# Kernel optimization log

Measured on AMD Instinct MI355X. Metric: run time of the kernel, lower is better.

Reference implementation:

```python
import jax, jax.numpy as jnp
import numpy as np

B, CIN, COUT, H, W, KH, KW, G = 16, 64, 128, 128, 128, 3, 3, 4


def setup_inputs() -> dict:
    key = jax.random.key(0)
    k1, k2, k3 = jax.random.split(key, 3)
    x = jax.random.normal(k1, (B, CIN, H, W), dtype=jnp.float32)
    spline_weights = jax.random.normal(k2, (COUT, CIN, KH, KW, G), dtype=jnp.float32)
    basis_weights = jax.random.normal(k3, (COUT, CIN, KH, KW), dtype=jnp.float32)
    return {"x": x, "spline_weights": spline_weights, "basis_weights": basis_weights}


def _conv_same(inp, w):
    # NCHW x OIHW -> NCHW, stride 1, SAME padding (pad = k//2, matches torch F.pad)
    return jax.lax.conv_general_dilated(
        inp, w, window_strides=(1, 1),
        padding=[(KH // 2, KH // 2), (KW // 2, KW // 2)],
        dimension_numbers=("NCHW", "OIHW", "NCHW"))


def reference(x, spline_weights, basis_weights):
    # spline branch: patch broadcast over grid then summed == conv with grid-summed kernel
    w_spline = spline_weights.sum(axis=-1)  # (COUT, CIN, KH, KW)
    # basis branch: silu applied to (zero-)padded patches; silu(0)=0 so equals conv(silu(x))
    return _conv_same(x, w_spline) + _conv_same(jax.nn.silu(x), basis_weights)
```

## Files before the change

kernel.cpp:

```cpp
#include <hip/hip_runtime.h>
#include <math.h>

#define B_    16
#define CIN   64
#define COUT  128
#define H_    128
#define W_    128
#define CI2   128
#define KTOT  1152

typedef __bf16 bf16x8 __attribute__((ext_vector_type(8)));
typedef float  f32x4  __attribute__((ext_vector_type(4)));

#define XT_BYTES  ((size_t)B_ * H_ * W_ * CI2 * 2)
#define WC_BYTES  ((size_t)COUT * KTOT * 2)
#define Z_OFF     (XT_BYTES + WC_BYTES)
#define WS_NEED   (Z_OFF + 4096)

__global__ __launch_bounds__(256) void w_prep(const float* __restrict__ sw,
                                              const float* __restrict__ bw,
                                              __bf16* __restrict__ wc,
                                              float* __restrict__ zp) {
    const int i = blockIdx.x * 256 + threadIdx.x;
    if (blockIdx.x == 0) zp[threadIdx.x] = 0.f;
    if (i >= COUT * KTOT) return;
    const int co = i / KTOT, k = i - co * KTOT;
    const int tap = k >> 7, ci2 = k & 127;
    float v;
    if (ci2 < CIN) {
        const float* p = sw + ((size_t)(co * CIN + ci2) * 9 + tap) * 4;
        v = p[0] + p[1] + p[2] + p[3];
    } else {
        v = bw[(size_t)(co * CIN + (ci2 - CIN)) * 9 + tap];
    }
    const int wm = co >> 6, m = (co >> 4) & 3, l15 = co & 15;
    const int ks = ci2 >> 5, lq = (ci2 >> 3) & 3, e = ci2 & 7;
    const int qq = (ks >> 1) * 18 + tap * 2 + (ks & 1);
    const int f  = wm * 4 + m;
    const size_t off = ((size_t)(qq * 8 + f)) * 512 + (lq * 16 + l15) * 8 + e;
    wc[off] = (__bf16)v;
}

__global__ __launch_bounds__(256) void xt_prep(const float* __restrict__ x,
                                               __bf16* __restrict__ xt) {
    __shared__ __align__(16) __bf16 tile[64][136];
    const int t  = threadIdx.x;
    const int w0 = blockIdx.x * 64;
    const int h  = blockIdx.y;
    const int b  = blockIdx.z;
    const float* xb = x + ((size_t)(b * CIN) * H_ + h) * W_ + w0;
#pragma unroll
    for (int rep = 0; rep < 16; ++rep) {
        const int idx = rep * 256 + t;
        const int ci = idx >> 6, w = idx & 63;
        const float v = xb[(size_t)ci * H_ * W_ + w];
        tile[w][ci]       = (__bf16)v;
        tile[w][CIN + ci] = (__bf16)(v / (1.f + __expf(-v)));
    }
    __syncthreads();
    __bf16* ob = xt + (((size_t)b * H_ + h) * W_ + w0) * CI2;
#pragma unroll
    for (int rep = 0; rep < 4; ++rep) {
        const int idx = rep * 256 + t;
        const int w = idx >> 4, sl = idx & 15;
        *(bf16x8*)(ob + (size_t)w * CI2 + sl * 8) = *(const bf16x8*)(&tile[w][sl * 8]);
    }
}

__global__ __launch_bounds__(256, 3) void kan_mfma(const __bf16* __restrict__ xt,
                                                   const __bf16* __restrict__ wc,
                                                   const float* __restrict__ zp,
                                                   float* __restrict__ out) {
    __shared__ __align__(16) char bh[1440 * 16];
    __shared__ __align__(16) char asA[512 * 16];
    __shared__ __align__(16) char asB[512 * 16];
    const int t    = threadIdx.x;
    const int lane = t & 63, wave = t >> 6;
    const int wm = wave >> 1, wn = wave & 1;
    const int l15 = lane & 15, lq = lane >> 4;

    const int orig = blockIdx.x;
    const int wid  = (orig & 7) * 256 + (orig >> 3);
    const int b  = wid >> 7;
    const int hy = (wid & 127) >> 3, wx = wid & 7;
    const int w0 = wx * 16, h0 = hy * 8;

    const size_t xbase = (size_t)b * (H_ * W_ * CI2);

#define STAGEB_(kk)                                                             \
    _Pragma("unroll")                                                           \
    for (int i = 0; i < 6; ++i) {                                               \
        const int s = i * 256 + t;                                              \
        if (s < 1440) {                                                         \
            const int pos = s >> 3, q = s & 7;                                  \
            const int ih = pos / 18, iw = pos - ih * 18;                        \
            const int gh = h0 + ih - 1, gw = w0 + iw - 1;                       \
            const int chunk = q ^ (pos & 7);                                    \
            const void* src;                                                    \
            if (gh >= 0 && gh < H_ && gw >= 0 && gw < W_)                       \
                src = (const void*)(xt + xbase +                                \
                      ((size_t)(gh * W_ + gw)) * CI2 + (kk) * 64 + chunk * 8);  \
            else                                                                \
                src = (const void*)zp;                                          \
            __builtin_amdgcn_global_load_lds(                                   \
                (const __attribute__((address_space(1))) unsigned int*)src,     \
                (__attribute__((address_space(3))) unsigned int*)(bh + s * 16), \
                16, 0, 0);                                                      \
        }                                                                       \
    }

#define STAGEQ_(buf, qq)                                                        \
    _Pragma("unroll")                                                           \
    for (int i = 0; i < 2; ++i) {                                               \
        const int s = i * 256 + t;                                              \
        __builtin_amdgcn_global_load_lds(                                       \
            (const __attribute__((address_space(1))) unsigned int*)              \
                (wc + (size_t)(qq) * 4096 + s * 8),                             \
            (__attribute__((address_space(3))) unsigned int*)((buf) + s * 16),  \
            16, 0, 0);                                                          \
    }

#define LOADB1_(dst, tp, ksl)                                                   \
    {                                                                           \
        const int kh_ = ((tp) * 11) >> 5;                                       \
        const int dp_ = kh_ * 18 + ((tp) - kh_ * 3);                            \
        _Pragma("unroll")                                                       \
        for (int n = 0; n < 4; ++n) {                                           \
            const int pos_ = pos0[n] + dp_;                                     \
            const int swz_ = ((ksl) * 4 + lq) ^ (pos_ & 7);                     \
            dst[n] = *(const bf16x8*)(bh + pos_ * 128 + swz_ * 16);             \
        }                                                                       \
    }

#define COMPUTE1_(buf, bfr)                                                     \
    {                                                                           \
        bf16x8 af[4];                                                           \
        _Pragma("unroll")                                                       \
        for (int m = 0; m < 4; ++m)                                             \
            af[m] = *(const bf16x8*)((buf) + (wm * 4 + m) * 1024 + lane * 16);  \
        __builtin_amdgcn_s_setprio(1);                                          \
        _Pragma("unroll")                                                       \
        for (int m = 0; m < 4; ++m)                                             \
            _Pragma("unroll")                                                   \
            for (int n = 0; n < 4; ++n)                                         \
                acc[m][n] = __builtin_amdgcn_mfma_f32_16x16x32_bf16(            \
                    af[m], bfr[n], acc[m][n], 0, 0, 0);                         \
        __builtin_amdgcn_s_setprio(0);                                          \
    }

    f32x4 acc[4][4] = {};
    int pos0[4];
#pragma unroll
    for (int n = 0; n < 4; ++n) pos0[n] = (wn * 4 + n) * 18 + l15;

    bf16x8 bP[4], bQ[4];

    STAGEB_(0);
    STAGEQ_(asA, 0);
    __syncthreads();
    LOADB1_(bP, 0, 0);

#pragma unroll 1
    for (int kk = 0; kk < 2; ++kk) {
        if (kk) {
            __syncthreads();
            STAGEB_(1);
            __syncthreads();
            LOADB1_(bP, 0, 0);
        }
#pragma unroll 1
        for (int tap = 0; tap < 9; ++tap) {
            const int qq = kk * 18 + tap * 2;
            if (qq + 1 < 36) STAGEQ_(asB, qq + 1);
            COMPUTE1_(asA, bP);
            LOADB1_(bQ, tap, 1);
            __syncthreads();
            if (qq + 2 < 36) STAGEQ_(asA, qq + 2);
            COMPUTE1_(asB, bQ);
            if (tap < 8) LOADB1_(bP, tap + 1, 0);
            __syncthreads();
        }
    }

    float* ob = out + (size_t)b * COUT * H_ * W_;
#pragma unroll
    for (int m = 0; m < 4; ++m) {
        const int co = wm * 64 + m * 16 + lq * 4;
#pragma unroll
        for (int n = 0; n < 4; ++n) {
            const int ph = wn * 4 + n;
            float* p = ob + ((size_t)co * H_ + (h0 + ph)) * W_ + (w0 + l15);
#pragma unroll
            for (int r = 0; r < 4; ++r)
                p[(size_t)r * H_ * W_] = acc[m][n][r];
        }
    }
#undef STAGEB_
#undef STAGEQ_
#undef LOADB1_
#undef COMPUTE1_
}

#define TS   16
#define COB  8
#define TIN  18
__global__ __launch_bounds__(256) void spline_sum_kernel(const float* __restrict__ sw,
                                                         float* __restrict__ wsum) {
    int i = blockIdx.x * 256 + threadIdx.x;
    if (i < COUT * CIN * 9) {
        const float4 v = *reinterpret_cast<const float4*>(sw + (size_t)i * 4);
        wsum[i] = v.x + v.y + v.z + v.w;
    }
}
__global__ __launch_bounds__(256) void kan_conv(const float* __restrict__ x,
                                                const float* __restrict__ wsp,
                                                const float* __restrict__ wb,
                                                float* __restrict__ out) {
    __shared__ float xsm[TIN][20];
    __shared__ float ssm[TIN][20];
    const int t = threadIdx.x, tx = t & 15, ty = t >> 4;
    const int w0 = (blockIdx.x & 7) * TS, h0 = (blockIdx.x >> 3) * TS;
    const int co0 = blockIdx.y * COB, b = blockIdx.z;
    float acc[COB];
#pragma unroll
    for (int i = 0; i < COB; ++i) acc[i] = 0.f;
    const float* xb = x + (size_t)b * CIN * H_ * W_;
    for (int ci = 0; ci < CIN; ++ci) {
        __syncthreads();
        const float* xc = xb + (size_t)ci * H_ * W_;
        for (int p = t; p < TIN * TIN; p += 256) {
            int r = p / TIN, c = p - r * TIN;
            int ih = h0 + r - 1, iw = w0 + c - 1;
            float v = 0.f;
            if (ih >= 0 && ih < H_ && iw >= 0 && iw < W_) v = xc[ih * W_ + iw];
            xsm[r][c] = v;
            ssm[r][c] = v / (1.f + expf(-v));
        }
        __syncthreads();
        float xv[9], sv[9];
#pragma unroll
        for (int kh = 0; kh < 3; ++kh)
#pragma unroll
            for (int kw = 0; kw < 3; ++kw) {
                xv[kh * 3 + kw] = xsm[ty + kh][tx + kw];
                sv[kh * 3 + kw] = ssm[ty + kh][tx + kw];
            }
#pragma unroll
        for (int co = 0; co < COB; ++co) {
            const float* w1 = wsp + ((size_t)(co0 + co) * CIN + ci) * 9;
            const float* w2 = wb  + ((size_t)(co0 + co) * CIN + ci) * 9;
#pragma unroll
            for (int k = 0; k < 9; ++k)
                acc[co] += xv[k] * w1[k] + sv[k] * w2[k];
        }
    }
    const int oh = h0 + ty, ow = w0 + tx;
#pragma unroll
    for (int co = 0; co < COB; ++co)
        out[(((size_t)b * COUT + (co0 + co)) * H_ + oh) * W_ + ow] = acc[co];
}

extern "C" void kernel_launch(void* const* d_in, const int* in_sizes, int n_in,
                              void* d_out, int out_size, void* d_ws, size_t ws_size,
                              hipStream_t stream) {
    const float* x  = (const float*)d_in[0];
    const float* sw = (const float*)d_in[1];
    const float* bw = (const float*)d_in[2];
    float* out = (float*)d_out;

    if (ws_size >= WS_NEED) {
        __bf16* xt = (__bf16*)d_ws;
        __bf16* wc = (__bf16*)((char*)d_ws + XT_BYTES);
        float*  zp = (float*)((char*)d_ws + Z_OFF);
        w_prep<<<(COUT * KTOT + 255) / 256, 256, 0, stream>>>(sw, bw, wc, zp);
        xt_prep<<<dim3(2, H_, B_), 256, 0, stream>>>(x, xt);
        kan_mfma<<<dim3(2048), 256, 0, stream>>>(xt, wc, zp, out);
    } else {
        float* wsum = (float*)d_ws;
        spline_sum_kernel<<<(COUT * CIN * 9 + 255) / 256, 256, 0, stream>>>(sw, wsum);
        kan_conv<<<dim3(64, COUT / COB, B_), 256, 0, stream>>>(x, wsum, bw, out);
    }
}
```

Before: 103.6 us.

## Triple-buffer weight staging with one barrier per K-step and partial vmcnt waits

Adds a third LDS buffer for weight tiles and fully unrolls the 36-step K loop. Each step now stages two steps ahead, waits only for older global loads via s_waitcnt vmcnt(2), and uses a single barrier instead of two __syncthreads per pair of steps. The aim is to overlap global-to-LDS loads with the MFMA work and cut synchronisation stalls. The extra 8 KB of LDS per block may lower occupancy under the 3-blocks-per-CU launch bound, and the hand-written vmcnt counts depend on how many loads STAGEQ_ issues per step.

```diff
diff --git a/kernel.cpp b/kernel.cpp
--- a/kernel.cpp
+++ b/kernel.cpp
@@ -74,6 +74,7 @@
     __shared__ __align__(16) char bh[1440 * 16];
     __shared__ __align__(16) char asA[512 * 16];
     __shared__ __align__(16) char asB[512 * 16];
+    __shared__ __align__(16) char asC[512 * 16];
     const int t    = threadIdx.x;
     const int lane = t & 63, wave = t >> 6;
     const int wm = wave >> 1, wn = wave & 1;
@@ -148,6 +149,13 @@
         __builtin_amdgcn_s_setprio(0);                                          \
     }
 
+#define PH2_(Q, CUR, STG, BU, BV)                                               \
+    STAGEQ_(STG, (Q) + 2);                                                      \
+    COMPUTE1_(CUR, BU);                                                         \
+    LOADB1_(BV, (((Q) + 1) % 18) >> 1, ((Q) + 1) & 1);                          \
+    asm volatile("s_waitcnt vmcnt(2)" ::: "memory");                            \
+    __builtin_amdgcn_s_barrier();
+
     f32x4 acc[4][4] = {};
     int pos0[4];
 #pragma unroll
@@ -157,30 +165,61 @@
 
     STAGEB_(0);
     STAGEQ_(asA, 0);
-    __syncthreads();
+    STAGEQ_(asB, 1);
+    asm volatile("s_waitcnt vmcnt(2)" ::: "memory");
+    __builtin_amdgcn_s_barrier();
     LOADB1_(bP, 0, 0);
 
-#pragma unroll 1
-    for (int kk = 0; kk < 2; ++kk) {
-        if (kk) {
-            __syncthreads();
-            STAGEB_(1);
-            __syncthreads();
-            LOADB1_(bP, 0, 0);
-        }
-#pragma unroll 1
-        for (int tap = 0; tap < 9; ++tap) {
-            const int qq = kk * 18 + tap * 2;
-            if (qq + 1 < 36) STAGEQ_(asB, qq + 1);
-            COMPUTE1_(asA, bP);
-            LOADB1_(bQ, tap, 1);
-            __syncthreads();
-            if (qq + 2 < 36) STAGEQ_(asA, qq + 2);
-            COMPUTE1_(asB, bQ);
-            if (tap < 8) LOADB1_(bP, tap + 1, 0);
-            __syncthreads();
-        }
-    }
+    PH2_( 0, asA, asC, bP, bQ)
+    PH2_( 1, asB, asA, bQ, bP)
+    PH2_( 2, asC, asB, bP, bQ)
+    PH2_( 3, asA, asC, bQ, bP)
+    PH2_( 4, asB, asA, bP, bQ)
+    PH2_( 5, asC, asB, bQ, bP)
+    PH2_( 6, asA, asC, bP, bQ)
+    PH2_( 7, asB, asA, bQ, bP)
+    PH2_( 8, asC, asB, bP, bQ)
+    PH2_( 9, asA, asC, bQ, bP)
+    PH2_(10, asB, asA, bP, bQ)
+    PH2_(11, asC, asB, bQ, bP)
+    PH2_(12, asA, asC, bP, bQ)
+    PH2_(13, asB, asA, bQ, bP)
+    PH2_(14, asC, asB, bP, bQ)
+    PH2_(15, asA, asC, bQ, bP)
+    PH2_(16, asB, asA, bP, bQ)
+
+    STAGEQ_(asB, 19);
+    COMPUTE1_(asC, bQ);
+    asm volatile("s_waitcnt vmcnt(0)" ::: "memory");
+    __builtin_amdgcn_s_barrier();
+    STAGEB_(1);
+    asm volatile("s_waitcnt vmcnt(0)" ::: "memory");
+    __builtin_amdgcn_s_barrier();
+    LOADB1_(bP, 0, 0);
+
+    PH2_(18, asA, asC, bP, bQ)
+    PH2_(19, asB, asA, bQ, bP)
+    PH2_(20, asC, asB, bP, bQ)
+    PH2_(21, asA, asC, bQ, bP)
+    PH2_(22, asB, asA, bP, bQ)
+    PH2_(23, asC, asB, bQ, bP)
+    PH2_(24, asA, asC, bP, bQ)
+    PH2_(25, asB, asA, bQ, bP)
+    PH2_(26, asC, asB, bP, bQ)
+    PH2_(27, asA, asC, bQ, bP)
+    PH2_(28, asB, asA, bP, bQ)
+    PH2_(29, asC, asB, bQ, bP)
+    PH2_(30, asA, asC, bP, bQ)
+    PH2_(31, asB, asA, bQ, bP)
+    PH2_(32, asC, asB, bP, bQ)
+    PH2_(33, asA, asC, bQ, bP)
+
+    COMPUTE1_(asB, bP);
+    LOADB1_(bQ, 8, 1);
+    asm volatile("s_waitcnt vmcnt(0)" ::: "memory");
+    __builtin_amdgcn_s_barrier();
+
+    COMPUTE1_(asC, bQ);
 
     float* ob = out + (size_t)b * COUT * H_ * W_;
 #pragma unroll
@@ -199,6 +238,7 @@
 #undef STAGEQ_
 #undef LOADB1_
 #undef COMPUTE1_
+#undef PH2_
 }
 
 #define TS   16
```

Measured after the change: 116.0 us. +11.9%, slower.

## Triple-buffer weight staging with single barrier per phase and partial vmcnt waits

Applied to the files above, without the earlier changes.

Adds a third LDS buffer for the weight (A) tiles so each stage is prefetched two steps ahead. The two barriers per tap pair become one barrier per phase, preceded by a partial s_waitcnt vmcnt(2) so the newest global loads can stay in flight across the barrier. This aims to hide global-load latency behind the MFMA work and cut synchronisation stalls. The cost is 8 KB more LDS per block, which may lower occupancy under launch_bounds(256,3), plus hand-scheduled wait counts that must match exactly how many loads STAGEQ issues.

```diff
diff --git a/kernel.cpp b/kernel.cpp
--- a/kernel.cpp
+++ b/kernel.cpp
@@ -74,6 +74,7 @@
     __shared__ __align__(16) char bh[1440 * 16];
     __shared__ __align__(16) char asA[512 * 16];
     __shared__ __align__(16) char asB[512 * 16];
+    __shared__ __align__(16) char asC[512 * 16];
     const int t    = threadIdx.x;
     const int lane = t & 63, wave = t >> 6;
     const int wm = wave >> 1, wn = wave & 1;
@@ -148,6 +149,17 @@
         __builtin_amdgcn_s_setprio(0);                                          \
     }
 
+#define PHASE_(CUR, STG, BU, BV, Q)                                             \
+    STAGEQ_(STG, (Q) + 2);                                                      \
+    COMPUTE1_(CUR, BU);                                                         \
+    {                                                                           \
+        const int q1_ = (Q) + 1;                                                \
+        const int qh_ = (q1_ >= 18) ? (q1_ - 18) : q1_;                         \
+        LOADB1_(BV, qh_ >> 1, qh_ & 1);                                         \
+    }                                                                           \
+    asm volatile("s_waitcnt vmcnt(2)" ::: "memory");                            \
+    __builtin_amdgcn_s_barrier();
+
     f32x4 acc[4][4] = {};
     int pos0[4];
 #pragma unroll
@@ -157,30 +169,55 @@
 
     STAGEB_(0);
     STAGEQ_(asA, 0);
-    __syncthreads();
+    STAGEQ_(asB, 1);
+    asm volatile("s_waitcnt vmcnt(2)" ::: "memory");
+    __builtin_amdgcn_s_barrier();
     LOADB1_(bP, 0, 0);
 
 #pragma unroll 1
-    for (int kk = 0; kk < 2; ++kk) {
-        if (kk) {
-            __syncthreads();
-            STAGEB_(1);
-            __syncthreads();
-            LOADB1_(bP, 0, 0);
-        }
+    for (int q = 0; q < 12; q += 6) {
+        PHASE_(asA, asC, bP, bQ, q)
+        PHASE_(asB, asA, bQ, bP, q + 1)
+        PHASE_(asC, asB, bP, bQ, q + 2)
+        PHASE_(asA, asC, bQ, bP, q + 3)
+        PHASE_(asB, asA, bP, bQ, q + 4)
+        PHASE_(asC, asB, bQ, bP, q + 5)
+    }
+    PHASE_(asA, asC, bP, bQ, 12)
+    PHASE_(asB, asA, bQ, bP, 13)
+    PHASE_(asC, asB, bP, bQ, 14)
+    PHASE_(asA, asC, bQ, bP, 15)
+    PHASE_(asB, asA, bP, bQ, 16)
+
+    STAGEQ_(asB, 19);
+    COMPUTE1_(asC, bQ);
+    asm volatile("s_waitcnt vmcnt(0)" ::: "memory");
+    __builtin_amdgcn_s_barrier();
+    STAGEB_(1);
+    asm volatile("s_waitcnt vmcnt(0)" ::: "memory");
+    __builtin_amdgcn_s_barrier();
+    LOADB1_(bP, 0, 0);
+
 #pragma unroll 1
-        for (int tap = 0; tap < 9; ++tap) {
-            const int qq = kk * 18 + tap * 2;
-            if (qq + 1 < 36) STAGEQ_(asB, qq + 1);
-            COMPUTE1_(asA, bP);
-            LOADB1_(bQ, tap, 1);
-            __syncthreads();
-            if (qq + 2 < 36) STAGEQ_(asA, qq + 2);
-            COMPUTE1_(asB, bQ);
-            if (tap < 8) LOADB1_(bP, tap + 1, 0);
-            __syncthreads();
-        }
-    }
+    for (int q = 18; q < 30; q += 6) {
+        PHASE_(asA, asC, bP, bQ, q)
+        PHASE_(asB, asA, bQ, bP, q + 1)
+        PHASE_(asC, asB, bP, bQ, q + 2)
+        PHASE_(asA, asC, bQ, bP, q + 3)
+        PHASE_(asB, asA, bP, bQ, q + 4)
+        PHASE_(asC, asB, bQ, bP, q + 5)
+    }
+    PHASE_(asA, asC, bP, bQ, 30)
+    PHASE_(asB, asA, bQ, bP, 31)
+    PHASE_(asC, asB, bP, bQ, 32)
+    PHASE_(asA, asC, bQ, bP, 33)
+
+    COMPUTE1_(asB, bP);
+    LOADB1_(bQ, 8, 1);
+    asm volatile("s_waitcnt vmcnt(0)" ::: "memory");
+    __builtin_amdgcn_s_barrier();
+
+    COMPUTE1_(asC, bQ);
 
     float* ob = out + (size_t)b * COUT * H_ * W_;
 #pragma unroll
@@ -199,6 +236,7 @@
 #undef STAGEQ_
 #undef LOADB1_
 #undef COMPUTE1_
+#undef PHASE_
 }
 
 #define TS   16
```

New measurement: 110.3 us. +6.5%, slower.

## Enlarge MFMA conv tile to 8x32 pixels with per-wave full COUT

Applied to the files above, without the earlier changes.

The output tile per block doubles from 8x16 to 8x32 pixels and the grid halves. Each wave now covers all 128 output channels over two output rows, using 8x4 accumulators, instead of a 64-channel by 4-row slice. The change is meant to cut halo overhead and weight-staging traffic per output and to raise MFMA work per LDS load. In exchange it doubles accumulator registers and LDS use, lowers launch bounds occupancy from 3 to 2 blocks, and drops the register prefetch of B fragments, so LDS reads are no longer overlapped with MFMAs.

```diff
diff --git a/kernel.cpp b/kernel.cpp
--- a/kernel.cpp
+++ b/kernel.cpp
@@ -33,10 +33,9 @@
     } else {
         v = bw[(size_t)(co * CIN + (ci2 - CIN)) * 9 + tap];
     }
-    const int wm = co >> 6, m = (co >> 4) & 3, l15 = co & 15;
+    const int f = co >> 4, l15 = co & 15;
     const int ks = ci2 >> 5, lq = (ci2 >> 3) & 3, e = ci2 & 7;
     const int qq = (ks >> 1) * 18 + tap * 2 + (ks & 1);
-    const int f  = wm * 4 + m;
     const size_t off = ((size_t)(qq * 8 + f)) * 512 + (lq * 16 + l15) * 8 + e;
     wc[off] = (__bf16)v;
 }
@@ -67,35 +66,34 @@
     }
 }
 
-__global__ __launch_bounds__(256, 3) void kan_mfma(const __bf16* __restrict__ xt,
+__global__ __launch_bounds__(256, 2) void kan_mfma(const __bf16* __restrict__ xt,
                                                    const __bf16* __restrict__ wc,
                                                    const float* __restrict__ zp,
                                                    float* __restrict__ out) {
-    __shared__ __align__(16) char bh[1440 * 16];
+    __shared__ __align__(16) char bh[2720 * 16];
     __shared__ __align__(16) char asA[512 * 16];
     __shared__ __align__(16) char asB[512 * 16];
     const int t    = threadIdx.x;
-    const int lane = t & 63, wave = t >> 6;
-    const int wm = wave >> 1, wn = wave & 1;
+    const int lane = t & 63, wn = t >> 6;
     const int l15 = lane & 15, lq = lane >> 4;
 
     const int orig = blockIdx.x;
-    const int wid  = (orig & 7) * 256 + (orig >> 3);
-    const int b  = wid >> 7;
-    const int hy = (wid & 127) >> 3, wx = wid & 7;
-    const int w0 = wx * 16, h0 = hy * 8;
+    const int wid  = (orig & 7) * 128 + (orig >> 3);
+    const int b  = wid >> 6;
+    const int hy = (wid >> 2) & 15, wx = wid & 3;
+    const int w0 = wx * 32, h0 = hy * 8;
 
     const size_t xbase = (size_t)b * (H_ * W_ * CI2);
 
 #define STAGEB_(kk)                                                             \
     _Pragma("unroll")                                                           \
-    for (int i = 0; i < 6; ++i) {                                               \
+    for (int i = 0; i < 11; ++i) {                                              \
         const int s = i * 256 + t;                                              \
-        if (s < 1440) {                                                         \
-            const int pos = s >> 3, q = s & 7;                                  \
-            const int ih = pos / 18, iw = pos - ih * 18;                        \
+        if (s < 2720) {                                                         \
+            const int cell = s >> 3, q = s & 7;                                 \
+            const int ih = cell / 34, iw = cell - ih * 34;                      \
             const int gh = h0 + ih - 1, gw = w0 + iw - 1;                       \
-            const int chunk = q ^ (pos & 7);                                    \
+            const int chunk = q ^ (cell & 7);                                   \
             const void* src;                                                    \
             if (gh >= 0 && gh < H_ && gw >= 0 && gw < W_)                       \
                 src = (const void*)(xt + xbase +                                \
@@ -120,76 +118,64 @@
             16, 0, 0);                                                          \
     }
 
-#define LOADB1_(dst, tp, ksl)                                                   \
+#define COMPUTE_(buf, tp, ksl)                                                  \
     {                                                                           \
         const int kh_ = ((tp) * 11) >> 5;                                       \
-        const int dp_ = kh_ * 18 + ((tp) - kh_ * 3);                            \
+        const int kw_ = (tp) - kh_ * 3;                                         \
+        bf16x8 af[8], bf[4];                                                    \
+        _Pragma("unroll")                                                       \
+        for (int m = 0; m < 8; ++m)                                             \
+            af[m] = *(const bf16x8*)((buf) + m * 1024 + lane * 16);             \
         _Pragma("unroll")                                                       \
         for (int n = 0; n < 4; ++n) {                                           \
-            const int pos_ = pos0[n] + dp_;                                     \
-            const int swz_ = ((ksl) * 4 + lq) ^ (pos_ & 7);                     \
-            dst[n] = *(const bf16x8*)(bh + pos_ * 128 + swz_ * 16);             \
+            const int cell = (wn * 2 + (n >> 1) + kh_) * 34 +                   \
+                             (n & 1) * 16 + l15 + kw_;                          \
+            const int swz  = ((ksl) * 4 + lq) ^ (cell & 7);                     \
+            bf[n] = *(const bf16x8*)(bh + cell * 128 + swz * 16);               \
         }                                                                       \
-    }
-
-#define COMPUTE1_(buf, bfr)                                                     \
-    {                                                                           \
-        bf16x8 af[4];                                                           \
-        _Pragma("unroll")                                                       \
-        for (int m = 0; m < 4; ++m)                                             \
-            af[m] = *(const bf16x8*)((buf) + (wm * 4 + m) * 1024 + lane * 16);  \
         __builtin_amdgcn_s_setprio(1);                                          \
         _Pragma("unroll")                                                       \
-        for (int m = 0; m < 4; ++m)                                             \
+        for (int m = 0; m < 8; ++m)                                             \
             _Pragma("unroll")                                                   \
             for (int n = 0; n < 4; ++n)                                         \
                 acc[m][n] = __builtin_amdgcn_mfma_f32_16x16x32_bf16(            \
-                    af[m], bfr[n], acc[m][n], 0, 0, 0);                         \
+                    af[m], bf[n], acc[m][n], 0, 0, 0);                          \
         __builtin_amdgcn_s_setprio(0);                                          \
     }
 
-    f32x4 acc[4][4] = {};
-    int pos0[4];
-#pragma unroll
-    for (int n = 0; n < 4; ++n) pos0[n] = (wn * 4 + n) * 18 + l15;
-
-    bf16x8 bP[4], bQ[4];
+    f32x4 acc[8][4] = {};
 
     STAGEB_(0);
     STAGEQ_(asA, 0);
     __syncthreads();
-    LOADB1_(bP, 0, 0);
 
 #pragma unroll 1
     for (int kk = 0; kk < 2; ++kk) {
         if (kk) {
-            __syncthreads();
             STAGEB_(1);
             __syncthreads();
-            LOADB1_(bP, 0, 0);
         }
 #pragma unroll 1
         for (int tap = 0; tap < 9; ++tap) {
             const int qq = kk * 18 + tap * 2;
-            if (qq + 1 < 36) STAGEQ_(asB, qq + 1);
-            COMPUTE1_(asA, bP);
-            LOADB1_(bQ, tap, 1);
+            STAGEQ_(asB, qq + 1);
+            COMPUTE_(asA, tap, 0);
             __syncthreads();
-            if (qq + 2 < 36) STAGEQ_(asA, qq + 2);
-            COMPUTE1_(asB, bQ);
-            if (tap < 8) LOADB1_(bP, tap + 1, 0);
+            if (kk == 0 || tap < 8) STAGEQ_(asA, qq + 2);
+            COMPUTE_(asB, tap, 1);
             __syncthreads();
         }
     }
 
     float* ob = out + (size_t)b * COUT * H_ * W_;
 #pragma unroll
-    for (int m = 0; m < 4; ++m) {
-        const int co = wm * 64 + m * 16 + lq * 4;
+    for (int m = 0; m < 8; ++m) {
+        const int co = m * 16 + lq * 4;
 #pragma unroll
         for (int n = 0; n < 4; ++n) {
-            const int ph = wn * 4 + n;
-            float* p = ob + ((size_t)co * H_ + (h0 + ph)) * W_ + (w0 + l15);
+            const int oh = h0 + wn * 2 + (n >> 1);
+            const int ow = w0 + (n & 1) * 16 + l15;
+            float* p = ob + ((size_t)co * H_ + oh) * W_ + ow;
 #pragma unroll
             for (int r = 0; r < 4; ++r)
                 p[(size_t)r * H_ * W_] = acc[m][n][r];
@@ -197,8 +183,7 @@
     }
 #undef STAGEB_
 #undef STAGEQ_
-#undef LOADB1_
-#undef COMPUTE1_
+#undef COMPUTE_
 }
 
 #define TS   16
@@ -274,7 +259,7 @@
         float*  zp = (float*)((char*)d_ws + Z_OFF);
         w_prep<<<(COUT * KTOT + 255) / 256, 256, 0, stream>>>(sw, bw, wc, zp);
         xt_prep<<<dim3(2, H_, B_), 256, 0, stream>>>(x, xt);
-        kan_mfma<<<dim3(2048), 256, 0, stream>>>(xt, wc, zp, out);
+        kan_mfma<<<dim3(1024), 256, 0, stream>>>(xt, wc, zp, out);
     } else {
         float* wsum = (float*)d_ws;
         spline_sum_kernel<<<(COUT * CIN * 9 + 255) / 256, 256, 0, stream>>>(sw, wsum);
```

Result: faster. 100.7 us (-2.8%).
